# Performance work log

Hardware: AMD Instinct MI355X
Metric: run time of the kernel (lower is better)

## Reference

```python
import jax, jax.numpy as jnp
import numpy as np

# Graph geometry: L depth levels of M nodes, fan_in K scalar connections, per-node dim D
L, M, K, D, B = 8, 128, 32, 16, 2048
N = L * M  # 1024 nodes


def setup_inputs() -> dict:
    key = jax.random.key(0)
    ks = jax.random.split(key, 6)
    x = jax.random.normal(ks[0], (B, D), jnp.float32)
    trace = jax.random.normal(ks[1], (N, B, D), jnp.float32)  # previous-step recurrent state per node
    src_node = jax.random.randint(ks[2], (N, K), 0, N + 1)    # 0 = external input x, else node id (1..N)
    src_feat = jax.random.randint(ks[3], (N, K), 0, D)        # scalar index k within source output
    W = jax.random.normal(ks[4], (N, D, K), jnp.float32) / np.sqrt(K)  # per-node Linear(K -> D)
    b = jax.random.normal(ks[5], (N, D), jnp.float32) * 0.01
    return {"x": x, "trace": trace, "src_node": src_node, "src_feat": src_feat, "W": W, "b": b}


def reference(x, trace, src_node, src_feat, W, b):
    # state buffers have row 0 = external input x, rows 1..N = node states
    h_state = jnp.concatenate([jnp.zeros((1, B, D), x.dtype), jax.lax.stop_gradient(trace)], axis=0)  # prev-step snapshot (detached, like torch .detach())
    cur0 = jnp.concatenate([x[None], jax.lax.stop_gradient(trace)], axis=0)  # current-step buffer, row 0 readable as input
    sn = src_node.reshape(L, M, K)
    sf = src_feat.reshape(L, M, K)
    Wl = W.reshape(L, M, D, K)
    bl = b.reshape(L, M, D)

    def step(cur, xs):
        l, sn_l, sf_l, W_l, b_l = xs
        g_cur = cur[sn_l, :, sf_l]      # [M, K, B] gather from current-step buffer
        g_h = h_state[sn_l, :, sf_l]    # [M, K, B] gather from previous-step snapshot
        # source depth >= current depth -> recurrent edge -> read h; else feedforward -> read cur
        use_h = (sn_l > 0) & (((sn_l - 1) // M) >= l)
        g = jnp.where(use_h[:, :, None], g_h, g_cur)                     # [M, K, B]
        o = jax.nn.relu(jnp.einsum('mkb,mdk->mbd', g, W_l) + b_l[:, None, :])  # [M, B, D]
        cur = jax.lax.dynamic_update_slice(cur, o, (1 + l * M, 0, 0))    # scatter into trace buffer
        return cur, o

    _, outs = jax.lax.scan(step, cur0, (jnp.arange(L), sn, sf, Wl, bl))  # outs: [L, M, B, D]
    return outs.reshape(N, B, D)  # updated trace; last node's forward return is outs[-1]
```

## Files before the change

kernel.cpp:

```cpp
#include <hip/hip_runtime.h>
#include <hip/hip_bf16.h>
#include <stdint.h>

#define L_ 8
#define M_ 128
#define K_ 32
#define D_ 16
#define B_ 2048
#define N_ 1024
#define SLAB_ 32768

#define WSF_XT    0u
#define WSF_TRT   32768u
#define WSF_OUTT  (32768u + 33554432u)
#define WSF_WT    (WSF_OUTT + 29360128u)
#define WSF_TOTAL (WSF_WT + 524288u)
#define WS_NEED_BYTES ((size_t)WSF_TOTAL * 4 + (size_t)N_ * K_ * 4)


__global__ __launch_bounds__(512) void prep6_kernel(const float* __restrict__ W,
                                                    const int* __restrict__ sn,
                                                    const int* __restrict__ sf,
                                                    float* __restrict__ wsf) {
    int n = blockIdx.x;
    int t = threadIdx.x;
    int d = t >> 5;
    int k = t & 31;
    wsf[WSF_WT + (size_t)n * 512 + k * 16 + d] = W[(size_t)n * 512 + t];
    if (t < K_) {
        int s = sn[(size_t)n * K_ + t];
        int f = sf[(size_t)n * K_ + t];
        int l = n >> 7;
        uint32_t off;
        if (s == 0) {
            off = WSF_XT + (uint32_t)(f * B_);
        } else if (s > (l << 7)) {
            off = WSF_TRT + (uint32_t)((s - 1) * SLAB_ + f * B_);
        } else {
            off = WSF_OUTT + (uint32_t)((s - 1) * SLAB_ + f * B_);
        }
        int mloc = n & 127;
        int mh   = mloc >> 6;
        int m6   = mloc & 63;
        uint32_t* meta = (uint32_t*)(wsf + WSF_TOTAL);
        meta[((uint32_t)((l << 1) + mh) << 11) + (uint32_t)((t << 6) + m6)] = off;
    }
}

__global__ __launch_bounds__(1024) void layer6_kernel(
    int l, float* __restrict__ wsf, const float* __restrict__ bias,
    float* __restrict__ out)
{
    extern __shared__ float G[];

    int tid = threadIdx.x;
    int mh  = blockIdx.x & 1;
    int bt  = blockIdx.x >> 1;
    int b0  = bt << 4;

    const uint32_t* mpl = (const uint32_t*)(wsf + WSF_TOTAL)
                        + (((uint32_t)(l << 1) + mh) << 11);

    {
        float4 gv[8];
#pragma unroll
        for (int jj = 0; jj < 8; ++jj) {
            uint32_t off = mpl[(jj << 8) + (tid >> 2)];
            gv[jj] = *((const float4*)(wsf + off + b0) + (tid & 3));
        }
        float4* G4 = (float4*)G;
#pragma unroll
        for (int jj = 0; jj < 8; ++jj) {
            G4[(jj << 10) + tid] = gv[jj];
        }
    }
    __syncthreads();

    int m6 = tid >> 4;
    int dq = (tid >> 2) & 3;
    int bq = tid & 3;
    int n  = (l << 7) + (mh << 6) + m6;

    float4 bv = *(const float4*)(bias + ((size_t)n << 4) + (dq << 2));
    float a00 = bv.x, a01 = bv.x, a02 = bv.x, a03 = bv.x;
    float a10 = bv.y, a11 = bv.y, a12 = bv.y, a13 = bv.y;
    float a20 = bv.z, a21 = bv.z, a22 = bv.z, a23 = bv.z;
    float a30 = bv.w, a31 = bv.w, a32 = bv.w, a33 = bv.w;

    const float4* wb = (const float4*)(wsf + WSF_WT + ((size_t)n << 9)) + dq;
    const float*  gk = G + (m6 << 4) + (bq << 2);
#pragma unroll
    for (int k = 0; k < K_; ++k) {
        float4 g4 = *(const float4*)(gk + (k << 10));
        float4 w  = wb[k << 2];
        a00 = fmaf(g4.x, w.x, a00); a01 = fmaf(g4.y, w.x, a01);
        a02 = fmaf(g4.z, w.x, a02); a03 = fmaf(g4.w, w.x, a03);
        a10 = fmaf(g4.x, w.y, a10); a11 = fmaf(g4.y, w.y, a11);
        a12 = fmaf(g4.z, w.y, a12); a13 = fmaf(g4.w, w.y, a13);
        a20 = fmaf(g4.x, w.z, a20); a21 = fmaf(g4.y, w.z, a21);
        a22 = fmaf(g4.z, w.z, a22); a23 = fmaf(g4.w, w.z, a23);
        a30 = fmaf(g4.x, w.w, a30); a31 = fmaf(g4.y, w.w, a31);
        a32 = fmaf(g4.z, w.w, a32); a33 = fmaf(g4.w, w.w, a33);
    }
    a00 = fmaxf(a00, 0.f); a01 = fmaxf(a01, 0.f); a02 = fmaxf(a02, 0.f); a03 = fmaxf(a03, 0.f);
    a10 = fmaxf(a10, 0.f); a11 = fmaxf(a11, 0.f); a12 = fmaxf(a12, 0.f); a13 = fmaxf(a13, 0.f);
    a20 = fmaxf(a20, 0.f); a21 = fmaxf(a21, 0.f); a22 = fmaxf(a22, 0.f); a23 = fmaxf(a23, 0.f);
    a30 = fmaxf(a30, 0.f); a31 = fmaxf(a31, 0.f); a32 = fmaxf(a32, 0.f); a33 = fmaxf(a33, 0.f);

    {
        float* op = out + ((((size_t)n << 11) + b0 + (bq << 2)) << 4) + (dq << 2);
        *(float4*)(op)      = make_float4(a00, a10, a20, a30);
        *(float4*)(op + 16) = make_float4(a01, a11, a21, a31);
        *(float4*)(op + 32) = make_float4(a02, a12, a22, a32);
        *(float4*)(op + 48) = make_float4(a03, a13, a23, a33);
    }

    if (l < L_ - 1) {
        float* tp = wsf + WSF_OUTT + ((size_t)n << 15) + ((size_t)(dq << 2)) * B_
                  + b0 + (bq << 2);
        *(float4*)(tp)          = make_float4(a00, a01, a02, a03);
        *(float4*)(tp + B_)     = make_float4(a10, a11, a12, a13);
        *(float4*)(tp + 2 * B_) = make_float4(a20, a21, a22, a23);
        *(float4*)(tp + 3 * B_) = make_float4(a30, a31, a32, a33);
    }
}


__global__ __launch_bounds__(256) void transpose_bd(const float* __restrict__ trace,
                                                    const float* __restrict__ x,
                                                    float* __restrict__ traceT,
                                                    float* __restrict__ xT) {
    int blk = blockIdx.x;
    const float* src;
    float* dst;
    int bt;
    if (blk < N_ * 32) {
        int n = blk >> 5;
        src = trace + (size_t)n * SLAB_;
        dst = traceT + (size_t)n * SLAB_;
        bt  = blk & 31;
    } else {
        src = x;
        dst = xT;
        bt  = blk - N_ * 32;
    }
    int b0 = bt * 64;

    __shared__ float lds[D_][65];

    int tid = threadIdx.x;
    const float4* s4 = (const float4*)src;
    int b  = tid >> 2;
    int dq = tid & 3;
    float4 v = s4[(size_t)(b0 + b) * 4 + dq];
    lds[dq * 4 + 0][b] = v.x;
    lds[dq * 4 + 1][b] = v.y;
    lds[dq * 4 + 2][b] = v.z;
    lds[dq * 4 + 3][b] = v.w;
    __syncthreads();

    int d  = tid >> 4;
    int bq = tid & 15;
    float4 w;
    w.x = lds[d][bq * 4 + 0];
    w.y = lds[d][bq * 4 + 1];
    w.z = lds[d][bq * 4 + 2];
    w.w = lds[d][bq * 4 + 3];
    ((float4*)(dst + (size_t)d * B_ + b0))[bq] = w;
}


__global__ __launch_bounds__(256) void layer_kernel(
    int l,
    const float* __restrict__ xbuf, int xfs, int xbs,
    const float* __restrict__ tbuf, int tfs, int tbs,
    const float* __restrict__ obuf, int ofs, int obs,
    const int* __restrict__ sn, const int* __restrict__ sf,
    const float* __restrict__ W, const float* __restrict__ bias,
    float* __restrict__ out, float* __restrict__ outT, int writeT)
{
    int m  = blockIdx.x >> 3;
    int bt = blockIdx.x & 7;
    int n  = l * M_ + m;
    int b  = bt * 256 + threadIdx.x;

    __shared__ float        Wsh[D_][K_];
    __shared__ float        bsh[D_];
    __shared__ const float* colp[K_];
    __shared__ int          colbs[K_];
    __shared__ float        osh[256][17];

    int tid = threadIdx.x;

    if (tid < 128) {
        ((float4*)&Wsh[0][0])[tid] = ((const float4*)(W + (size_t)n * D_ * K_))[tid];
    }
    if (tid < D_) bsh[tid] = bias[(size_t)n * D_ + tid];
    if (tid < K_) {
        int s = sn[(size_t)n * K_ + tid];
        int f = sf[(size_t)n * K_ + tid];
        const float* p;
        int bs;
        if (s == 0) {
            p  = xbuf + (size_t)f * xfs;
            bs = xbs;
        } else {
            int ls = (s - 1) >> 7;
            if (ls >= l) {
                p  = tbuf + (size_t)(s - 1) * SLAB_ + (size_t)f * tfs;
                bs = tbs;
            } else {
                p  = obuf + (size_t)(s - 1) * SLAB_ + (size_t)f * ofs;
                bs = obs;
            }
        }
        colp[tid]  = p;
        colbs[tid] = bs;
    }
    __syncthreads();

    float g[K_];
#pragma unroll
    for (int k = 0; k < K_; ++k) {
        g[k] = colp[k][(size_t)b * colbs[k]];
    }

#pragma unroll
    for (int d = 0; d < D_; ++d) {
        float acc = bsh[d];
#pragma unroll
        for (int k = 0; k < K_; ++k) acc = fmaf(g[k], Wsh[d][k], acc);
        acc = fmaxf(acc, 0.0f);
        osh[tid][d] = acc;
        if (writeT) outT[(size_t)n * SLAB_ + (size_t)d * B_ + b] = acc;
    }
    __syncthreads();

    float4* region4 = (float4*)(out + (size_t)n * SLAB_ + (size_t)(bt * 256) * D_);
#pragma unroll
    for (int j = 0; j < 4; ++j) {
        int i   = j * 256 + tid;
        int row = i >> 2;
        int c0  = (i & 3) * 4;
        float4 w;
        w.x = osh[row][c0 + 0];
        w.y = osh[row][c0 + 1];
        w.z = osh[row][c0 + 2];
        w.w = osh[row][c0 + 3];
        region4[i] = w;
    }
}

extern "C" void kernel_launch(void* const* d_in, const int* in_sizes, int n_in,
                              void* d_out, int out_size, void* d_ws, size_t ws_size,
                              hipStream_t stream) {
    const float* x     = (const float*)d_in[0];
    const float* trace = (const float*)d_in[1];
    const int*   sn    = (const int*)d_in[2];
    const int*   sf    = (const int*)d_in[3];
    const float* W     = (const float*)d_in[4];
    const float* bias  = (const float*)d_in[5];
    float*       out   = (float*)d_out;

    static int use_fused = -1;
    if (use_fused < 0) {
        hipError_t e = hipFuncSetAttribute(
            reinterpret_cast<const void*>(layer6_kernel),
            hipFuncAttributeMaxDynamicSharedMemorySize, 131072);
        if (e != hipSuccess) {
            (void)hipGetLastError();
            use_fused = 0;
        } else {
            use_fused = 1;
        }
    }

    if (use_fused == 1 && ws_size >= WS_NEED_BYTES) {
        float* wsf = (float*)d_ws;
        transpose_bd<<<N_ * 32 + 32, 256, 0, stream>>>(trace, x,
                                                       wsf + WSF_TRT, wsf + WSF_XT);
        prep6_kernel<<<N_, 512, 0, stream>>>(W, sn, sf, wsf);
        for (int l = 0; l < L_; ++l) {
            layer6_kernel<<<256, 1024, 131072, stream>>>(l, wsf, bias, out);
        }
        return;
    }

    const size_t xT_elems  = (size_t)D_ * B_;
    const size_t big_elems = (size_t)N_ * SLAB_;
    const size_t needA = sizeof(float) * (xT_elems + 2 * big_elems);
    const size_t needB = sizeof(float) * (xT_elems + 1 * big_elems);

    float* ws = (float*)d_ws;

    if (ws_size >= needA) {
        float* xT     = ws;
        float* traceT = ws + xT_elems;
        float* outT   = traceT + big_elems;

        transpose_bd<<<N_ * 32 + 32, 256, 0, stream>>>(trace, x, traceT, xT);
        for (int l = 0; l < L_; ++l) {
            layer_kernel<<<M_ * 8, 256, 0, stream>>>(
                l,
                xT,     B_, 1,
                traceT, B_, 1,
                outT,   B_, 1,
                sn, sf, W, bias, out, outT, 1);
        }
    } else if (ws_size >= needB) {
        float* xT     = ws;
        float* traceT = ws + xT_elems;

        transpose_bd<<<N_ * 32 + 32, 256, 0, stream>>>(trace, x, traceT, xT);
        for (int l = 0; l < L_; ++l) {
            layer_kernel<<<M_ * 8, 256, 0, stream>>>(
                l,
                xT,     B_, 1,
                traceT, B_, 1,
                out,    1,  D_,
                sn, sf, W, bias, out, nullptr, 0);
        }
    } else {
        for (int l = 0; l < L_; ++l) {
            layer_kernel<<<M_ * 8, 256, 0, stream>>>(
                l,
                x,     1, D_,
                trace, 1, D_,
                out,   1, D_,
                sn, sf, W, bias, out, nullptr, 0);
        }
    }
}
```

Before: 407.2 us.

## Fuse transpose, prep and all layers into one cooperative persistent kernel

Replaces the transpose kernel, the prep kernel and the eight per-layer launches with a single cooperative kernel of 256 blocks of 1024 threads. The stages are separated by grid-wide syncs instead of kernel boundaries. The final output stores switch to nontemporal stores. The aim is to remove launch overhead and inter-kernel gaps. In exchange the kernel now depends on cooperative-launch co-residency with 128KB of LDS per block, and it runs the transpose phase with fewer resident threads.

```diff
diff --git a/kernel.cpp b/kernel.cpp
--- a/kernel.cpp
+++ b/kernel.cpp
@@ -1,6 +1,9 @@
 #include <hip/hip_runtime.h>
 #include <hip/hip_bf16.h>
+#include <hip/hip_cooperative_groups.h>
 #include <stdint.h>
+
+namespace cg = cooperative_groups;
 
 #define L_ 8
 #define M_ 128
@@ -10,12 +13,179 @@
 #define N_ 1024
 #define SLAB_ 32768
 
+typedef float nfloat4 __attribute__((ext_vector_type(4)));
+
 #define WSF_XT    0u
 #define WSF_TRT   32768u
 #define WSF_OUTT  (32768u + 33554432u)
 #define WSF_WT    (WSF_OUTT + 29360128u)
 #define WSF_TOTAL (WSF_WT + 524288u)
 #define WS_NEED_BYTES ((size_t)WSF_TOTAL * 4 + (size_t)N_ * K_ * 4)
+
+
+__global__ __launch_bounds__(1024) void mega_kernel(
+    const float* __restrict__ x, const float* __restrict__ trace,
+    const int* __restrict__ sn, const int* __restrict__ sf,
+    const float* __restrict__ W, const float* __restrict__ bias,
+    float* __restrict__ wsf, float* __restrict__ out)
+{
+    extern __shared__ float G[];
+    cg::grid_group grid = cg::this_grid();
+
+    int tid = threadIdx.x;
+    int bid = blockIdx.x;
+
+    {
+        int eng = (bid << 2) + (tid >> 8);
+        int t   = tid & 255;
+        float* lds = G + (tid >> 8) * 1040;
+        int b  = t >> 2;
+        int dq = t & 3;
+        int d  = t >> 4;
+        int bq = t & 15;
+        for (int i = 0; i < 33; ++i) {
+            int blk = (i << 10) + eng;
+            bool active = blk < N_ * 32 + 32;
+            const float* src = nullptr;
+            float* dst = nullptr;
+            int bt = 0;
+            if (active) {
+                if (blk < N_ * 32) {
+                    int n = blk >> 5;
+                    src = trace + (size_t)n * SLAB_;
+                    dst = wsf + WSF_TRT + (size_t)n * SLAB_;
+                    bt  = blk & 31;
+                } else {
+                    src = x;
+                    dst = wsf + WSF_XT;
+                    bt  = blk - N_ * 32;
+                }
+                int b0 = bt * 64;
+                float4 v = ((const float4*)src)[(size_t)(b0 + b) * 4 + dq];
+                lds[(dq * 4 + 0) * 65 + b] = v.x;
+                lds[(dq * 4 + 1) * 65 + b] = v.y;
+                lds[(dq * 4 + 2) * 65 + b] = v.z;
+                lds[(dq * 4 + 3) * 65 + b] = v.w;
+            }
+            __syncthreads();
+            if (active) {
+                int b0 = bt * 64;
+                float4 w4;
+                w4.x = lds[d * 65 + bq * 4 + 0];
+                w4.y = lds[d * 65 + bq * 4 + 1];
+                w4.z = lds[d * 65 + bq * 4 + 2];
+                w4.w = lds[d * 65 + bq * 4 + 3];
+                ((float4*)(dst + (size_t)d * B_ + b0))[bq] = w4;
+            }
+            __syncthreads();
+        }
+    }
+
+    {
+        uint32_t* meta = (uint32_t*)(wsf + WSF_TOTAL);
+        for (int it = 0; it < 2; ++it) {
+            int n = (bid << 2) + (it << 1) + (tid >> 9);
+            int t = tid & 511;
+            int d = t >> 5;
+            int k = t & 31;
+            wsf[WSF_WT + (size_t)n * 512 + k * 16 + d] = W[(size_t)n * 512 + t];
+            if (t < K_) {
+                int s = sn[(size_t)n * K_ + t];
+                int f = sf[(size_t)n * K_ + t];
+                int l = n >> 7;
+                uint32_t off;
+                if (s == 0) {
+                    off = WSF_XT + (uint32_t)(f * B_);
+                } else if (s > (l << 7)) {
+                    off = WSF_TRT + (uint32_t)((s - 1) * SLAB_ + f * B_);
+                } else {
+                    off = WSF_OUTT + (uint32_t)((s - 1) * SLAB_ + f * B_);
+                }
+                int mloc = n & 127;
+                meta[((uint32_t)((l << 1) + (mloc >> 6)) << 11)
+                     + (uint32_t)((t << 6) + (mloc & 63))] = off;
+            }
+        }
+    }
+
+    grid.sync();
+
+    int bt2 = bid & 127;
+    int mh  = bid >> 7;
+    int b0  = bt2 << 4;
+    const uint32_t* metab = (const uint32_t*)(wsf + WSF_TOTAL);
+
+    int m6  = tid >> 4;
+    int dq2 = (tid >> 2) & 3;
+    int bq2 = tid & 3;
+
+    for (int l = 0; l < L_; ++l) {
+        const uint32_t* mpl = metab + (((uint32_t)(l << 1) + mh) << 11);
+
+        float4 gv[8];
+#pragma unroll
+        for (int jj = 0; jj < 8; ++jj) {
+            uint32_t off = mpl[(jj << 8) + (tid >> 2)];
+            gv[jj] = *((const float4*)(wsf + off + b0) + (tid & 3));
+        }
+        float4* G4 = (float4*)G;
+#pragma unroll
+        for (int jj = 0; jj < 8; ++jj) {
+            G4[(jj << 10) + tid] = gv[jj];
+        }
+        __syncthreads();
+
+        int n = (l << 7) + (mh << 6) + m6;
+
+        float4 bv = *(const float4*)(bias + ((size_t)n << 4) + (dq2 << 2));
+        float a00 = bv.x, a01 = bv.x, a02 = bv.x, a03 = bv.x;
+        float a10 = bv.y, a11 = bv.y, a12 = bv.y, a13 = bv.y;
+        float a20 = bv.z, a21 = bv.z, a22 = bv.z, a23 = bv.z;
+        float a30 = bv.w, a31 = bv.w, a32 = bv.w, a33 = bv.w;
+
+        const float4* wb = (const float4*)(wsf + WSF_WT + ((size_t)n << 9)) + dq2;
+        const float*  gk = G + (m6 << 4) + (bq2 << 2);
+#pragma unroll
+        for (int k = 0; k < K_; ++k) {
+            float4 g4 = *(const float4*)(gk + (k << 10));
+            float4 w  = wb[k << 2];
+            a00 = fmaf(g4.x, w.x, a00); a01 = fmaf(g4.y, w.x, a01);
+            a02 = fmaf(g4.z, w.x, a02); a03 = fmaf(g4.w, w.x, a03);
+            a10 = fmaf(g4.x, w.y, a10); a11 = fmaf(g4.y, w.y, a11);
+            a12 = fmaf(g4.z, w.y, a12); a13 = fmaf(g4.w, w.y, a13);
+            a20 = fmaf(g4.x, w.z, a20); a21 = fmaf(g4.y, w.z, a21);
+            a22 = fmaf(g4.z, w.z, a22); a23 = fmaf(g4.w, w.z, a23);
+            a30 = fmaf(g4.x, w.w, a30); a31 = fmaf(g4.y, w.w, a31);
+            a32 = fmaf(g4.z, w.w, a32); a33 = fmaf(g4.w, w.w, a33);
+        }
+        a00 = fmaxf(a00, 0.f); a01 = fmaxf(a01, 0.f); a02 = fmaxf(a02, 0.f); a03 = fmaxf(a03, 0.f);
+        a10 = fmaxf(a10, 0.f); a11 = fmaxf(a11, 0.f); a12 = fmaxf(a12, 0.f); a13 = fmaxf(a13, 0.f);
+        a20 = fmaxf(a20, 0.f); a21 = fmaxf(a21, 0.f); a22 = fmaxf(a22, 0.f); a23 = fmaxf(a23, 0.f);
+        a30 = fmaxf(a30, 0.f); a31 = fmaxf(a31, 0.f); a32 = fmaxf(a32, 0.f); a33 = fmaxf(a33, 0.f);
+
+        {
+            float* op = out + ((((size_t)n << 11) + b0 + (bq2 << 2)) << 4) + (dq2 << 2);
+            nfloat4 v0 = {a00, a10, a20, a30};
+            nfloat4 v1 = {a01, a11, a21, a31};
+            nfloat4 v2 = {a02, a12, a22, a32};
+            nfloat4 v3 = {a03, a13, a23, a33};
+            __builtin_nontemporal_store(v0, (nfloat4*)(op));
+            __builtin_nontemporal_store(v1, (nfloat4*)(op + 16));
+            __builtin_nontemporal_store(v2, (nfloat4*)(op + 32));
+            __builtin_nontemporal_store(v3, (nfloat4*)(op + 48));
+        }
+
+        if (l < L_ - 1) {
+            float* tp = wsf + WSF_OUTT + ((size_t)n << 15) + ((size_t)(dq2 << 2)) * B_
+                      + b0 + (bq2 << 2);
+            *(float4*)(tp)          = make_float4(a00, a01, a02, a03);
+            *(float4*)(tp + B_)     = make_float4(a10, a11, a12, a13);
+            *(float4*)(tp + 2 * B_) = make_float4(a20, a21, a22, a23);
+            *(float4*)(tp + 3 * B_) = make_float4(a30, a31, a32, a33);
+            grid.sync();
+        }
+    }
+}
 
 
 __global__ __launch_bounds__(512) void prep6_kernel(const float* __restrict__ W,
@@ -125,7 +295,6 @@
     }
 }
 
-
 __global__ __launch_bounds__(256) void transpose_bd(const float* __restrict__ trace,
                                                     const float* __restrict__ x,
                                                     float* __restrict__ traceT,
@@ -262,21 +431,34 @@
     const float* bias  = (const float*)d_in[5];
     float*       out   = (float*)d_out;
 
-    static int use_fused = -1;
-    if (use_fused < 0) {
-        hipError_t e = hipFuncSetAttribute(
+    static int mode = -1;
+    if (mode < 0) {
+        hipError_t e1 = hipFuncSetAttribute(
+            reinterpret_cast<const void*>(mega_kernel),
+            hipFuncAttributeMaxDynamicSharedMemorySize, 131072);
+        hipError_t e2 = hipFuncSetAttribute(
             reinterpret_cast<const void*>(layer6_kernel),
             hipFuncAttributeMaxDynamicSharedMemorySize, 131072);
-        if (e != hipSuccess) {
+        (void)hipGetLastError();
+        if (e1 == hipSuccess)      mode = 2;
+        else if (e2 == hipSuccess) mode = 1;
+        else                       mode = 0;
+    }
+
+    if (mode >= 1 && ws_size >= WS_NEED_BYTES) {
+        float* wsf = (float*)d_ws;
+
+        if (mode == 2) {
+            void* args[] = {(void*)&x, (void*)&trace, (void*)&sn, (void*)&sf,
+                            (void*)&W, (void*)&bias, (void*)&wsf, (void*)&out};
+            hipError_t e = hipLaunchCooperativeKernel(
+                reinterpret_cast<const void*>(mega_kernel),
+                dim3(256), dim3(1024), args, 131072u, stream);
+            if (e == hipSuccess) return;
             (void)hipGetLastError();
-            use_fused = 0;
-        } else {
-            use_fused = 1;
-        }
-    }
-
-    if (use_fused == 1 && ws_size >= WS_NEED_BYTES) {
-        float* wsf = (float*)d_ws;
+            mode = 1;
+        }
+
         transpose_bd<<<N_ * 32 + 32, 256, 0, stream>>>(trace, x,
                                                        wsf + WSF_TRT, wsf + WSF_XT);
         prep6_kernel<<<N_, 512, 0, stream>>>(W, sn, sf, wsf);
```

Measured after the change: 665.5 us. +63.5%, slower.
